# Kernel optimization log

Measured on AMD Instinct MI355X. Metric: run time of the kernel, lower is better.

The kernel has to match this reference:

```python
import jax, jax.numpy as jnp
import numpy as np

N_HEAD = 16
D_HEAD = 64


def setup_inputs() -> dict:
    key = jax.random.key(0)
    k1, k2, k3 = jax.random.split(key, 3)
    B, L, D = 2, 2048, 1024
    inp = jax.random.normal(k1, (B, L, D), dtype=jnp.float32)
    # causal mask: True -> masked (matches torch masked_fill_ semantics)
    mask = jnp.triu(jnp.ones((L, L), dtype=bool), k=1)[None, None, :, :]
    W_qkv = jax.random.normal(k2, (D, 3 * N_HEAD * D_HEAD), dtype=jnp.float32) * 0.02
    b_qkv = jnp.zeros((3 * N_HEAD * D_HEAD,), dtype=jnp.float32)
    W_out = jax.random.normal(k3, (N_HEAD * D_HEAD, D), dtype=jnp.float32) * 0.02
    b_out = jnp.zeros((D,), dtype=jnp.float32)
    return {"input": inp, "mask": mask, "W_qkv": W_qkv, "b_qkv": b_qkv,
            "W_out": W_out, "b_out": b_out}


def reference(input, mask, W_qkv, b_qkv, W_out, b_out):
    B, L, D = input.shape
    qkv = input @ W_qkv + b_qkv                       # [B, L, 3*H*Dh]
    q, k, v = jnp.split(qkv, 3, axis=-1)              # each [B, L, H*Dh]
    qh = q.reshape(B, L, N_HEAD, D_HEAD)
    kh = k.reshape(B, L, N_HEAD, D_HEAD)
    vh = v.reshape(B, L, N_HEAD, D_HEAD)
    scale = 1.0 / (D_HEAD ** 0.5)
    attn = jnp.einsum('bqhd,bkhd->bhqk', qh, kh) * scale  # [B, H, L, L]
    attn = jnp.where(mask, -jnp.inf, attn)
    attn = jax.nn.softmax(attn, axis=-1)
    out = jnp.einsum('bhqk,bkhd->bqhd', attn, vh).reshape(B, L, D)
    out = out @ W_out + b_out
    # next_memory equivalent: (k, v) pre-head-split, as in the torch code
    return (out, k, v)
```

## Files before the change

kernel.cpp:

```cpp
#include <hip/hip_runtime.h>
#include <cstdint>

#define NHEAD 16
#define DHEAD 64
#define SEQ   2048
#define DMODEL 1024
#define MTOT  4096
#define NQKV  3072

typedef __bf16 bf16x8 __attribute__((ext_vector_type(8)));
typedef short  s16x4  __attribute__((ext_vector_type(4)));
typedef float  f32x4  __attribute__((ext_vector_type(4)));

__device__ __forceinline__ unsigned short f2bf(float f) {
  union { float f; unsigned u; } v; v.f = f;
  unsigned r = v.u + 0x7fffu + ((v.u >> 16) & 1u);
  return (unsigned short)(r >> 16);
}

__device__ __forceinline__ void gl_lds16(const void* g, void* l) {
  __builtin_amdgcn_global_load_lds(
      reinterpret_cast<const __attribute__((address_space(1))) unsigned int*>(
          reinterpret_cast<uintptr_t>(g)),
      reinterpret_cast<__attribute__((address_space(3))) unsigned int*>(
          reinterpret_cast<uintptr_t>(l)),
      16, 0, 0);
}

#if __has_builtin(__builtin_amdgcn_mfma_f32_16x16x16bf16_1k)
#define MFMA_PV(a, b, c) __builtin_amdgcn_mfma_f32_16x16x16bf16_1k(a, b, c, 0, 0, 0)
#else
__device__ __forceinline__ f32x4 mfma_pv_asm(s16x4 a, s16x4 b, f32x4 c) {
  f32x4 d;
  asm volatile("v_mfma_f32_16x16x16_bf16 %0, %1, %2, %3"
               : "=v"(d) : "v"(a), "v"(b), "v"(c));
  return d;
}
#define MFMA_PV(a, b, c) mfma_pv_asm(a, b, c)
#endif

__global__ void k_prepass(const float* __restrict__ x, unsigned short* __restrict__ y,
                          const float* __restrict__ W0, unsigned short* __restrict__ T0,
                          const float* __restrict__ W1, unsigned short* __restrict__ T1) {
  __shared__ unsigned short t[32][33];
  const int bid = blockIdx.x;
  if (bid < 4096) {
    const int i = bid * 256 + threadIdx.x;
    float4 v = reinterpret_cast<const float4*>(x)[i];
    ushort4 o;
    o.x = f2bf(v.x); o.y = f2bf(v.y); o.z = f2bf(v.z); o.w = f2bf(v.w);
    reinterpret_cast<ushort4*>(y)[i] = o;
  } else {
    const int b2 = bid - 4096;
    const int bx = b2 & 127;
    const int by = b2 >> 7;
    const float* W = (bx < 96) ? W0 : W1;
    unsigned short* WT = (bx < 96) ? T0 : T1;
    const int N = (bx < 96) ? 3072 : 1024;
    const int n0 = ((bx < 96) ? bx : (bx - 96)) * 32;
    const int k0 = by * 32;
    const int tx = threadIdx.x & 31, ty = threadIdx.x >> 5;
    for (int i = ty; i < 32; i += 8)
      t[i][tx] = f2bf(W[(size_t)(k0 + i) * N + n0 + tx]);
    __syncthreads();
    for (int i = ty; i < 32; i += 8)
      WT[(size_t)(n0 + i) * 1024 + k0 + tx] = t[tx][i];
  }
}

__global__ __launch_bounds__(256, 3) void k_gemm_qkv(
    const unsigned short* __restrict__ A, const unsigned short* __restrict__ Bt,
    const float* __restrict__ bias, float* __restrict__ outbase,
    unsigned short* __restrict__ qbf, unsigned short* __restrict__ kbf,
    unsigned short* __restrict__ vtbf) {
  __shared__ __attribute__((aligned(16))) unsigned short As[2][128 * 32];
  __shared__ __attribute__((aligned(16))) unsigned short Bs[2][128 * 32];
  const int tid = threadIdx.x, lane = tid & 63;
  const int w = tid >> 6, wm = w >> 1, wn = w & 1;
  const int c = lane & 15, q = lane >> 4;
  const int kc = (c & 3) ^ ((c >> 2) & 3);
  const int bm = blockIdx.x * 128, bn = blockIdx.y * 128;
  const int srow = tid >> 2;
  const int skey = (srow & 3) ^ ((srow >> 2) & 3);
  const int scolsw = (((tid & 3) ^ skey) << 3);
  const unsigned short* Ag = A + (size_t)(bm + srow) * DMODEL + scolsw;
  const unsigned short* Bg = Bt + (size_t)(bn + srow) * DMODEL + scolsw;
  f32x4 acc[4][4] = {};

  gl_lds16(Ag, As[0] + tid * 8);
  gl_lds16(Ag + (size_t)64 * DMODEL, As[0] + 2048 + tid * 8);
  gl_lds16(Bg, Bs[0] + tid * 8);
  gl_lds16(Bg + (size_t)64 * DMODEL, Bs[0] + 2048 + tid * 8);

  for (int kt = 0; kt < 32; ++kt) {
    const int cur = kt & 1;
    __syncthreads();
    if (kt < 31) {
      const int k0 = (kt + 1) * 32;
      gl_lds16(Ag + k0, As[cur ^ 1] + tid * 8);
      gl_lds16(Ag + k0 + (size_t)64 * DMODEL, As[cur ^ 1] + 2048 + tid * 8);
      gl_lds16(Bg + k0, Bs[cur ^ 1] + tid * 8);
      gl_lds16(Bg + k0 + (size_t)64 * DMODEL, Bs[cur ^ 1] + 2048 + tid * 8);
    }
    const int ch = (q ^ kc) << 3;
    bf16x8 af[4], bfr[4];
#pragma unroll
    for (int i = 0; i < 4; ++i)
      af[i] = *reinterpret_cast<const bf16x8*>(As[cur] + (wm * 64 + i * 16 + c) * 32 + ch);
#pragma unroll
    for (int j = 0; j < 4; ++j)
      bfr[j] = *reinterpret_cast<const bf16x8*>(Bs[cur] + (wn * 64 + j * 16 + c) * 32 + ch);
#pragma unroll
    for (int i = 0; i < 4; ++i)
#pragma unroll
      for (int j = 0; j < 4; ++j)
        acc[i][j] = __builtin_amdgcn_mfma_f32_16x16x32_bf16(af[i], bfr[j], acc[i][j], 0, 0, 0);
  }

  const int sec = bn >> 10;
  if (sec == 2) {
    __syncthreads();
    char* stg = reinterpret_cast<char*>((w < 2) ? (&As[0][0] + w * 4096)
                                                : (&Bs[0][0] + (w - 2) * 4096));
#pragma unroll
    for (int j = 0; j < 4; ++j) {
      const int gn = bn + wn * 64 + j * 16 + c;
      const float bv = bias[gn];
      const int cc = gn & 1023;
      const int ln = j * 16 + c;
#pragma unroll
      for (int i = 0; i < 4; ++i) {
        const int gm0 = bm + wm * 64 + i * 16 + q * 4;
        const int lm0 = i * 16 + q * 4;
        float vals[4];
#pragma unroll
        for (int r = 0; r < 4; ++r) {
          vals[r] = acc[i][j][r] + bv;
          outbase[(size_t)8388608 + (size_t)(gm0 + r) * DMODEL + cc] = vals[r];
        }
        ushort4 tv;
        tv.x = f2bf(vals[0]); tv.y = f2bf(vals[1]);
        tv.z = f2bf(vals[2]); tv.w = f2bf(vals[3]);
        *reinterpret_cast<ushort4*>(stg + ln * 128 + ((lm0 * 2) ^ ((ln & 7) << 4))) = tv;
      }
    }
    const int gmb = bm + wm * 64;
    const int bb = gmb >> 11, tokb = gmb & 2047;
    const int hh = ((bn + wn * 64) >> 6) & 15;
    unsigned short* vrow = vtbf + ((size_t)(bb * NHEAD + hh) * DHEAD) * SEQ + tokb;
#pragma unroll
    for (int it = 0; it < 8; ++it) {
      const int r_ = (lane >> 3) + it * 8;
      const int g = lane & 7;
      const uint4 val = *reinterpret_cast<const uint4*>(
          stg + r_ * 128 + (((unsigned)g << 4) ^ ((r_ & 7) << 4)));
      *reinterpret_cast<uint4*>(vrow + (size_t)r_ * SEQ + g * 8) = val;
    }
  } else {
#pragma unroll
    for (int j = 0; j < 4; ++j) {
      const int gn = bn + wn * 64 + j * 16 + c;
      const float bv = bias[gn];
      const int cc = gn & 1023, hh = cc >> 6, dd = cc & 63;
#pragma unroll
      for (int i = 0; i < 4; ++i) {
#pragma unroll
        for (int r = 0; r < 4; ++r) {
          const int gm = bm + wm * 64 + i * 16 + q * 4 + r;
          const int bb = gm >> 11, tok = gm & 2047;
          const float val = acc[i][j][r] + bv;
          const size_t hoff = ((size_t)(bb * NHEAD + hh) * SEQ + tok) * DHEAD + dd;
          if (sec == 0) {
            qbf[hoff] = f2bf(val);
          } else {
            outbase[(size_t)4194304 + (size_t)gm * DMODEL + cc] = val;
            kbf[hoff] = f2bf(val);
          }
        }
      }
    }
  }
}

__global__ __launch_bounds__(256) void k_attn(
    const unsigned short* __restrict__ qbf, const unsigned short* __restrict__ kbf,
    const unsigned short* __restrict__ vtbf, unsigned short* __restrict__ aout) {
  __shared__ __attribute__((aligned(16))) unsigned short Ks[128 * 64];
  __shared__ __attribute__((aligned(16))) unsigned short Vs[64 * 128];

  const int tid = threadIdx.x, lane = tid & 63, w = tid >> 6;
  const int c = lane & 15, q = lane >> 4;
  const int oo = blockIdx.x >> 5, kk = oo & 7, ssl = oo >> 3;
  const int qsub = (ssl == 0) ? (31 - kk) : (ssl == 1) ? kk
                 : (ssl == 2) ? (23 - kk) : (8 + kk);
  const int bh = blockIdx.x & 31;
  const int kmax = qsub >> 1;
  const size_t hoff = (size_t)bh * SEQ * DHEAD;

  const unsigned short* qg = qbf + hoff + (size_t)(qsub * 64 + w * 16 + c) * DHEAD;
  const bf16x8 qb0 = *reinterpret_cast<const bf16x8*>(qg + q * 8);
  const bf16x8 qb1 = *reinterpret_cast<const bf16x8*>(qg + 32 + q * 8);

  f32x4 o[4] = {};
  float lpart = 0.f;
  const float sscale = 0.125f * 1.44269504088896340736f;
  const int qloc = (qsub & 1) * 64 + w * 16 + c;
  const int cx = c & 7;

  const int krow = tid >> 3, kswz = (tid & 7) ^ (krow & 7);
  const int vrow = tid >> 4, vswz = (tid & 15) ^ (vrow & 7);
  const unsigned short* kgb = kbf + hoff;
  const unsigned short* vgb = vtbf + (size_t)bh * DHEAD * SEQ;

  for (int kt = 0; kt <= kmax; ++kt) {
    __syncthreads();
    const unsigned short* kg = kgb + (size_t)kt * 128 * DHEAD;
#pragma unroll
    for (int is = 0; is < 4; ++is)
      gl_lds16(kg + (krow + is * 32) * 64 + kswz * 8, Ks + is * 2048 + tid * 8);
    const unsigned short* vg = vgb + kt * 128;
#pragma unroll
    for (int is = 0; is < 4; ++is)
      gl_lds16(vg + (size_t)(vrow + is * 16) * SEQ + vswz * 8, Vs + is * 2048 + tid * 8);
    __syncthreads();

    f32x4 s[8];
    __builtin_amdgcn_s_setprio(1);
#pragma unroll
    for (int mi = 0; mi < 8; ++mi) {
      const unsigned short* kr = Ks + (mi * 16 + c) * 64;
      const bf16x8 ak0 = *reinterpret_cast<const bf16x8*>(kr + (q ^ cx) * 8);
      const bf16x8 ak1 = *reinterpret_cast<const bf16x8*>(kr + ((4 + q) ^ cx) * 8);
      f32x4 t = {};
      t = __builtin_amdgcn_mfma_f32_16x16x32_bf16(ak0, qb0, t, 0, 0, 0);
      t = __builtin_amdgcn_mfma_f32_16x16x32_bf16(ak1, qb1, t, 0, 0, 0);
      s[mi] = t;
    }
    __builtin_amdgcn_s_setprio(0);

    if (kt == kmax) {
#pragma unroll
      for (int mi = 0; mi < 8; ++mi)
#pragma unroll
        for (int r = 0; r < 4; ++r)
          if (mi * 16 + q * 4 + r > qloc) s[mi][r] = -__builtin_inff();
    }

    s16x4 pb[8];
#pragma unroll
    for (int mi = 0; mi < 8; ++mi) {
      const float p0 = __builtin_amdgcn_exp2f(s[mi][0] * sscale);
      const float p1 = __builtin_amdgcn_exp2f(s[mi][1] * sscale);
      const float p2 = __builtin_amdgcn_exp2f(s[mi][2] * sscale);
      const float p3 = __builtin_amdgcn_exp2f(s[mi][3] * sscale);
      lpart += (p0 + p1) + (p2 + p3);
      union { s16x4 v; unsigned u[2]; } pk;
      pk.u[0] = __builtin_amdgcn_perm(__float_as_uint(p1), __float_as_uint(p0), 0x07060302u);
      pk.u[1] = __builtin_amdgcn_perm(__float_as_uint(p3), __float_as_uint(p2), 0x07060302u);
      pb[mi] = pk.v;
    }

    __builtin_amdgcn_s_setprio(1);
#pragma unroll
    for (int dm = 0; dm < 4; ++dm) {
      const unsigned short* vr = Vs + (dm * 16 + c) * 128 + (q & 1) * 4;
#pragma unroll
      for (int kf = 0; kf < 8; ++kf) {
        const s16x4 av = *reinterpret_cast<const s16x4*>(
            vr + (((kf * 2 + (q >> 1)) ^ cx) * 8));
        o[dm] = MFMA_PV(av, pb[kf], o[dm]);
      }
    }
    __builtin_amdgcn_s_setprio(0);
  }

  float lrun = lpart;
  lrun += __shfl_xor(lrun, 16);
  lrun += __shfl_xor(lrun, 32);

  const float linv = 1.0f / lrun;
  unsigned short* Ws = Ks + w * 1024;
#pragma unroll
  for (int dm = 0; dm < 4; ++dm) {
    ushort4 ov;
    ov.x = f2bf(o[dm][0] * linv);
    ov.y = f2bf(o[dm][1] * linv);
    ov.z = f2bf(o[dm][2] * linv);
    ov.w = f2bf(o[dm][3] * linv);
    const int bofs = c * 128 + ((dm * 32 + q * 8) ^ ((c & 7) << 4));
    *reinterpret_cast<ushort4*>(Ws + (bofs >> 1)) = ov;
  }
  const int b = bh >> 4, h = bh & 15;
#pragma unroll
  for (int it = 0; it < 2; ++it) {
    const int r_ = (lane >> 3) + it * 8;
    const int g = lane & 7;
    const uint4 val = *reinterpret_cast<const uint4*>(
        Ws + ((r_ * 128 + (((unsigned)g ^ (r_ & 7)) << 4)) >> 1));
    const int row = b * SEQ + qsub * 64 + w * 16 + r_;
    *reinterpret_cast<uint4*>(aout + (size_t)row * DMODEL + h * 64 + g * 8) = val;
  }
}

__global__ __launch_bounds__(256) void k_gemm_out(
    const unsigned short* __restrict__ A, const unsigned short* __restrict__ Bt,
    const float* __restrict__ bias, float* __restrict__ C) {
  __shared__ __attribute__((aligned(16))) unsigned short As[2][128 * 32];
  __shared__ __attribute__((aligned(16))) unsigned short Bs[2][64 * 32];
  const int tid = threadIdx.x, lane = tid & 63;
  const int w = tid >> 6, wm = w >> 1, wn = w & 1;
  const int c = lane & 15, q = lane >> 4;
  const int kc = (c & 3) ^ ((c >> 2) & 3);
  const int bm = blockIdx.x * 128, bn = blockIdx.y * 64;
  const int srow = tid >> 2;
  const int skey = (srow & 3) ^ ((srow >> 2) & 3);
  const int scolsw = (((tid & 3) ^ skey) << 3);
  const unsigned short* Ag = A + (size_t)(bm + srow) * DMODEL + scolsw;
  const unsigned short* Bg = Bt + (size_t)(bn + srow) * DMODEL + scolsw;
  f32x4 acc[4][2] = {};

  gl_lds16(Ag, As[0] + tid * 8);
  gl_lds16(Ag + (size_t)64 * DMODEL, As[0] + 2048 + tid * 8);
  gl_lds16(Bg, Bs[0] + tid * 8);

  for (int kt = 0; kt < 32; ++kt) {
    const int cur = kt & 1;
    __syncthreads();
    if (kt < 31) {
      const int k0 = (kt + 1) * 32;
      gl_lds16(Ag + k0, As[cur ^ 1] + tid * 8);
      gl_lds16(Ag + k0 + (size_t)64 * DMODEL, As[cur ^ 1] + 2048 + tid * 8);
      gl_lds16(Bg + k0, Bs[cur ^ 1] + tid * 8);
    }
    const int ch = (q ^ kc) << 3;
    bf16x8 af[4], bfr[2];
#pragma unroll
    for (int i = 0; i < 4; ++i)
      af[i] = *reinterpret_cast<const bf16x8*>(As[cur] + (wm * 64 + i * 16 + c) * 32 + ch);
#pragma unroll
    for (int j = 0; j < 2; ++j)
      bfr[j] = *reinterpret_cast<const bf16x8*>(Bs[cur] + (wn * 32 + j * 16 + c) * 32 + ch);
#pragma unroll
    for (int i = 0; i < 4; ++i)
#pragma unroll
      for (int j = 0; j < 2; ++j)
        acc[i][j] = __builtin_amdgcn_mfma_f32_16x16x32_bf16(af[i], bfr[j], acc[i][j], 0, 0, 0);
  }

#pragma unroll
  for (int j = 0; j < 2; ++j) {
    const int gn = bn + wn * 32 + j * 16 + c;
    const float bv = bias[gn];
#pragma unroll
    for (int i = 0; i < 4; ++i)
#pragma unroll
      for (int r = 0; r < 4; ++r) {
        const int gm = bm + wm * 64 + i * 16 + q * 4 + r;
        C[(size_t)gm * DMODEL + gn] = acc[i][j][r] + bv;
      }
  }
}

extern "C" void kernel_launch(void* const* d_in, const int* in_sizes, int n_in,
                              void* d_out, int out_size, void* d_ws, size_t ws_size,
                              hipStream_t stream) {
  (void)in_sizes; (void)n_in; (void)out_size; (void)ws_size;
  const float* input = (const float*)d_in[0];
  const float* W_qkv = (const float*)d_in[2];
  const float* b_qkv = (const float*)d_in[3];
  const float* W_out = (const float*)d_in[4];
  const float* b_out = (const float*)d_in[5];
  float* out = (float*)d_out;

  unsigned char* ws = (unsigned char*)d_ws;
  unsigned short* Abf   = (unsigned short*)(ws + 0);
  unsigned short* WqkvT = (unsigned short*)(ws + 8388608);
  unsigned short* WoutT = (unsigned short*)(ws + 14680064);
  unsigned short* Qbf   = (unsigned short*)(ws + 16777216);
  unsigned short* Kbf   = (unsigned short*)(ws + 25165824);
  unsigned short* VTbf  = (unsigned short*)(ws + 33554432);
  unsigned short* Aout  = (unsigned short*)(ws + 41943040);

  k_prepass<<<8192, 256, 0, stream>>>(input, Abf, W_qkv, WqkvT, W_out, WoutT);
  k_gemm_qkv<<<dim3(32, 24), 256, 0, stream>>>(Abf, WqkvT, b_qkv, out, Qbf, Kbf, VTbf);
  k_attn<<<1024, 256, 0, stream>>>(Qbf, Kbf, VTbf, Aout);
  k_gemm_out<<<dim3(32, 16), 256, 0, stream>>>(Aout, WoutT, b_out, out);
}
```

Before: 188.6 us.

## Pair mirrored causal query tiles per attention block to share K/V loads

```diff
diff --git a/kernel.cpp b/kernel.cpp
--- a/kernel.cpp
+++ b/kernel.cpp
@@ -38,6 +38,8 @@
 }
 #define MFMA_PV(a, b, c) mfma_pv_asm(a, b, c)
 #endif
+
+#define QSCALE 0.18033688011112042f
 
 __global__ void k_prepass(const float* __restrict__ x, unsigned short* __restrict__ y,
                           const float* __restrict__ W0, unsigned short* __restrict__ T0,
@@ -171,7 +173,7 @@
           const float val = acc[i][j][r] + bv;
           const size_t hoff = ((size_t)(bb * NHEAD + hh) * SEQ + tok) * DHEAD + dd;
           if (sec == 0) {
-            qbf[hoff] = f2bf(val);
+            qbf[hoff] = f2bf(val * QSCALE);
           } else {
             outbase[(size_t)4194304 + (size_t)gm * DMODEL + cc] = val;
             kbf[hoff] = f2bf(val);
@@ -190,21 +192,23 @@
 
   const int tid = threadIdx.x, lane = tid & 63, w = tid >> 6;
   const int c = lane & 15, q = lane >> 4;
-  const int oo = blockIdx.x >> 5, kk = oo & 7, ssl = oo >> 3;
-  const int qsub = (ssl == 0) ? (31 - kk) : (ssl == 1) ? kk
-                 : (ssl == 2) ? (23 - kk) : (8 + kk);
   const int bh = blockIdx.x & 31;
-  const int kmax = qsub >> 1;
+  const int jj = blockIdx.x >> 5;
+  const int qa = 31 - jj, qb = jj;
+  const int ka = qa >> 1, kb = qb >> 1;
   const size_t hoff = (size_t)bh * SEQ * DHEAD;
 
-  const unsigned short* qg = qbf + hoff + (size_t)(qsub * 64 + w * 16 + c) * DHEAD;
-  const bf16x8 qb0 = *reinterpret_cast<const bf16x8*>(qg + q * 8);
-  const bf16x8 qb1 = *reinterpret_cast<const bf16x8*>(qg + 32 + q * 8);
-
-  f32x4 o[4] = {};
-  float lpart = 0.f;
-  const float sscale = 0.125f * 1.44269504088896340736f;
-  const int qloc = (qsub & 1) * 64 + w * 16 + c;
+  const unsigned short* qga = qbf + hoff + (size_t)(qa * 64 + w * 16 + c) * DHEAD;
+  const bf16x8 qA0 = *reinterpret_cast<const bf16x8*>(qga + q * 8);
+  const bf16x8 qA1 = *reinterpret_cast<const bf16x8*>(qga + 32 + q * 8);
+  const unsigned short* qgb = qbf + hoff + (size_t)(qb * 64 + w * 16 + c) * DHEAD;
+  const bf16x8 qB0 = *reinterpret_cast<const bf16x8*>(qgb + q * 8);
+  const bf16x8 qB1 = *reinterpret_cast<const bf16x8*>(qgb + 32 + q * 8);
+
+  f32x4 oa[4] = {}, ob[4] = {};
+  float lpa = 0.f, lpb = 0.f;
+  const int qloca = (qa & 1) * 64 + w * 16 + c;
+  const int qlocb = (qb & 1) * 64 + w * 16 + c;
   const int cx = c & 7;
 
   const int krow = tid >> 3, kswz = (tid & 7) ^ (krow & 7);
@@ -212,7 +216,7 @@
   const unsigned short* kgb = kbf + hoff;
   const unsigned short* vgb = vtbf + (size_t)bh * DHEAD * SEQ;
 
-  for (int kt = 0; kt <= kmax; ++kt) {
+  for (int kt = 0; kt <= ka; ++kt) {
     __syncthreads();
     const unsigned short* kg = kgb + (size_t)kt * 128 * DHEAD;
 #pragma unroll
@@ -224,81 +228,160 @@
       gl_lds16(vg + (size_t)(vrow + is * 16) * SEQ + vswz * 8, Vs + is * 2048 + tid * 8);
     __syncthreads();
 
-    f32x4 s[8];
-    __builtin_amdgcn_s_setprio(1);
-#pragma unroll
-    for (int mi = 0; mi < 8; ++mi) {
-      const unsigned short* kr = Ks + (mi * 16 + c) * 64;
-      const bf16x8 ak0 = *reinterpret_cast<const bf16x8*>(kr + (q ^ cx) * 8);
-      const bf16x8 ak1 = *reinterpret_cast<const bf16x8*>(kr + ((4 + q) ^ cx) * 8);
-      f32x4 t = {};
-      t = __builtin_amdgcn_mfma_f32_16x16x32_bf16(ak0, qb0, t, 0, 0, 0);
-      t = __builtin_amdgcn_mfma_f32_16x16x32_bf16(ak1, qb1, t, 0, 0, 0);
-      s[mi] = t;
-    }
-    __builtin_amdgcn_s_setprio(0);
-
-    if (kt == kmax) {
-#pragma unroll
-      for (int mi = 0; mi < 8; ++mi)
-#pragma unroll
-        for (int r = 0; r < 4; ++r)
-          if (mi * 16 + q * 4 + r > qloc) s[mi][r] = -__builtin_inff();
-    }
-
-    s16x4 pb[8];
-#pragma unroll
-    for (int mi = 0; mi < 8; ++mi) {
-      const float p0 = __builtin_amdgcn_exp2f(s[mi][0] * sscale);
-      const float p1 = __builtin_amdgcn_exp2f(s[mi][1] * sscale);
-      const float p2 = __builtin_amdgcn_exp2f(s[mi][2] * sscale);
-      const float p3 = __builtin_amdgcn_exp2f(s[mi][3] * sscale);
-      lpart += (p0 + p1) + (p2 + p3);
-      union { s16x4 v; unsigned u[2]; } pk;
-      pk.u[0] = __builtin_amdgcn_perm(__float_as_uint(p1), __float_as_uint(p0), 0x07060302u);
-      pk.u[1] = __builtin_amdgcn_perm(__float_as_uint(p3), __float_as_uint(p2), 0x07060302u);
-      pb[mi] = pk.v;
-    }
-
-    __builtin_amdgcn_s_setprio(1);
+    {
+      f32x4 s[8];
+      __builtin_amdgcn_s_setprio(1);
+#pragma unroll
+      for (int mi = 0; mi < 8; ++mi) {
+        const unsigned short* kr = Ks + (mi * 16 + c) * 64;
+        const bf16x8 ak0 = *reinterpret_cast<const bf16x8*>(kr + (q ^ cx) * 8);
+        const bf16x8 ak1 = *reinterpret_cast<const bf16x8*>(kr + ((4 + q) ^ cx) * 8);
+        f32x4 t = {};
+        t = __builtin_amdgcn_mfma_f32_16x16x32_bf16(ak0, qA0, t, 0, 0, 0);
+        t = __builtin_amdgcn_mfma_f32_16x16x32_bf16(ak1, qA1, t, 0, 0, 0);
+        s[mi] = t;
+      }
+      __builtin_amdgcn_s_setprio(0);
+
+      if (kt == ka) {
+#pragma unroll
+        for (int mi = 0; mi < 8; ++mi)
+#pragma unroll
+          for (int r = 0; r < 4; ++r)
+            if (mi * 16 + q * 4 + r > qloca) s[mi][r] = -__builtin_inff();
+      }
+
+      s16x4 pb[8];
+#pragma unroll
+      for (int mi = 0; mi < 8; ++mi) {
+        const float p0 = __builtin_amdgcn_exp2f(s[mi][0]);
+        const float p1 = __builtin_amdgcn_exp2f(s[mi][1]);
+        const float p2 = __builtin_amdgcn_exp2f(s[mi][2]);
+        const float p3 = __builtin_amdgcn_exp2f(s[mi][3]);
+        lpa += (p0 + p1) + (p2 + p3);
+        union { s16x4 v; unsigned u[2]; } pk;
+        pk.u[0] = __builtin_amdgcn_perm(__float_as_uint(p1), __float_as_uint(p0), 0x07060302u);
+        pk.u[1] = __builtin_amdgcn_perm(__float_as_uint(p3), __float_as_uint(p2), 0x07060302u);
+        pb[mi] = pk.v;
+      }
+
+      __builtin_amdgcn_s_setprio(1);
+#pragma unroll
+      for (int dm = 0; dm < 4; ++dm) {
+        const unsigned short* vr = Vs + (dm * 16 + c) * 128 + (q & 1) * 4;
+#pragma unroll
+        for (int kf = 0; kf < 8; ++kf) {
+          const s16x4 av = *reinterpret_cast<const s16x4*>(
+              vr + (((kf * 2 + (q >> 1)) ^ cx) * 8));
+          oa[dm] = MFMA_PV(av, pb[kf], oa[dm]);
+        }
+      }
+      __builtin_amdgcn_s_setprio(0);
+    }
+
+    if (kt <= kb) {
+      f32x4 s[8];
+      __builtin_amdgcn_s_setprio(1);
+#pragma unroll
+      for (int mi = 0; mi < 8; ++mi) {
+        const unsigned short* kr = Ks + (mi * 16 + c) * 64;
+        const bf16x8 ak0 = *reinterpret_cast<const bf16x8*>(kr + (q ^ cx) * 8);
+        const bf16x8 ak1 = *reinterpret_cast<const bf16x8*>(kr + ((4 + q) ^ cx) * 8);
+        f32x4 t = {};
+        t = __builtin_amdgcn_mfma_f32_16x16x32_bf16(ak0, qB0, t, 0, 0, 0);
+        t = __builtin_amdgcn_mfma_f32_16x16x32_bf16(ak1, qB1, t, 0, 0, 0);
+        s[mi] = t;
+      }
+      __builtin_amdgcn_s_setprio(0);
+
+      if (kt == kb) {
+#pragma unroll
+        for (int mi = 0; mi < 8; ++mi)
+#pragma unroll
+          for (int r = 0; r < 4; ++r)
+            if (mi * 16 + q * 4 + r > qlocb) s[mi][r] = -__builtin_inff();
+      }
+
+      s16x4 pb[8];
+#pragma unroll
+      for (int mi = 0; mi < 8; ++mi) {
+        const float p0 = __builtin_amdgcn_exp2f(s[mi][0]);
+        const float p1 = __builtin_amdgcn_exp2f(s[mi][1]);
+        const float p2 = __builtin_amdgcn_exp2f(s[mi][2]);
+        const float p3 = __builtin_amdgcn_exp2f(s[mi][3]);
+        lpb += (p0 + p1) + (p2 + p3);
+        union { s16x4 v; unsigned u[2]; } pk;
+        pk.u[0] = __builtin_amdgcn_perm(__float_as_uint(p1), __float_as_uint(p0), 0x07060302u);
+        pk.u[1] = __builtin_amdgcn_perm(__float_as_uint(p3), __float_as_uint(p2), 0x07060302u);
+        pb[mi] = pk.v;
+      }
+
+      __builtin_amdgcn_s_setprio(1);
+#pragma unroll
+      for (int dm = 0; dm < 4; ++dm) {
+        const unsigned short* vr = Vs + (dm * 16 + c) * 128 + (q & 1) * 4;
+#pragma unroll
+        for (int kf = 0; kf < 8; ++kf) {
+          const s16x4 av = *reinterpret_cast<const s16x4*>(
+              vr + (((kf * 2 + (q >> 1)) ^ cx) * 8));
+          ob[dm] = MFMA_PV(av, pb[kf], ob[dm]);
+        }
+      }
+      __builtin_amdgcn_s_setprio(0);
+    }
+  }
+
+  float la = lpa; la += __shfl_xor(la, 16); la += __shfl_xor(la, 32);
+  float lb = lpb; lb += __shfl_xor(lb, 16); lb += __shfl_xor(lb, 32);
+
+  __syncthreads();
+  const int bidx = bh >> 4, h = bh & 15;
+
+  {
+    const float linv = 1.0f / la;
+    unsigned short* Ws = Ks + w * 2048;
 #pragma unroll
     for (int dm = 0; dm < 4; ++dm) {
-      const unsigned short* vr = Vs + (dm * 16 + c) * 128 + (q & 1) * 4;
-#pragma unroll
-      for (int kf = 0; kf < 8; ++kf) {
-        const s16x4 av = *reinterpret_cast<const s16x4*>(
-            vr + (((kf * 2 + (q >> 1)) ^ cx) * 8));
-        o[dm] = MFMA_PV(av, pb[kf], o[dm]);
-      }
-    }
-    __builtin_amdgcn_s_setprio(0);
-  }
-
-  float lrun = lpart;
-  lrun += __shfl_xor(lrun, 16);
-  lrun += __shfl_xor(lrun, 32);
-
-  const float linv = 1.0f / lrun;
-  unsigned short* Ws = Ks + w * 1024;
-#pragma unroll
-  for (int dm = 0; dm < 4; ++dm) {
-    ushort4 ov;
-    ov.x = f2bf(o[dm][0] * linv);
-    ov.y = f2bf(o[dm][1] * linv);
-    ov.z = f2bf(o[dm][2] * linv);
-    ov.w = f2bf(o[dm][3] * linv);
-    const int bofs = c * 128 + ((dm * 32 + q * 8) ^ ((c & 7) << 4));
-    *reinterpret_cast<ushort4*>(Ws + (bofs >> 1)) = ov;
-  }
-  const int b = bh >> 4, h = bh & 15;
-#pragma unroll
-  for (int it = 0; it < 2; ++it) {
-    const int r_ = (lane >> 3) + it * 8;
-    const int g = lane & 7;
-    const uint4 val = *reinterpret_cast<const uint4*>(
-        Ws + ((r_ * 128 + (((unsigned)g ^ (r_ & 7)) << 4)) >> 1));
-    const int row = b * SEQ + qsub * 64 + w * 16 + r_;
-    *reinterpret_cast<uint4*>(aout + (size_t)row * DMODEL + h * 64 + g * 8) = val;
+      ushort4 ov;
+      ov.x = f2bf(oa[dm][0] * linv);
+      ov.y = f2bf(oa[dm][1] * linv);
+      ov.z = f2bf(oa[dm][2] * linv);
+      ov.w = f2bf(oa[dm][3] * linv);
+      const int bofs = c * 128 + ((dm * 32 + q * 8) ^ ((c & 7) << 4));
+      *reinterpret_cast<ushort4*>(Ws + (bofs >> 1)) = ov;
+    }
+#pragma unroll
+    for (int it = 0; it < 2; ++it) {
+      const int r_ = (lane >> 3) + it * 8;
+      const int g = lane & 7;
+      const uint4 val = *reinterpret_cast<const uint4*>(
+          Ws + ((r_ * 128 + (((unsigned)g ^ (r_ & 7)) << 4)) >> 1));
+      const int row = bidx * SEQ + qa * 64 + w * 16 + r_;
+      *reinterpret_cast<uint4*>(aout + (size_t)row * DMODEL + h * 64 + g * 8) = val;
+    }
+  }
+  {
+    const float linv = 1.0f / lb;
+    unsigned short* Ws = Ks + w * 2048 + 1024;
+#pragma unroll
+    for (int dm = 0; dm < 4; ++dm) {
+      ushort4 ov;
+      ov.x = f2bf(ob[dm][0] * linv);
+      ov.y = f2bf(ob[dm][1] * linv);
+      ov.z = f2bf(ob[dm][2] * linv);
+      ov.w = f2bf(ob[dm][3] * linv);
+      const int bofs = c * 128 + ((dm * 32 + q * 8) ^ ((c & 7) << 4));
+      *reinterpret_cast<ushort4*>(Ws + (bofs >> 1)) = ov;
+    }
+#pragma unroll
+    for (int it = 0; it < 2; ++it) {
+      const int r_ = (lane >> 3) + it * 8;
+      const int g = lane & 7;
+      const uint4 val = *reinterpret_cast<const uint4*>(
+          Ws + ((r_ * 128 + (((unsigned)g ^ (r_ & 7)) << 4)) >> 1));
+      const int row = bidx * SEQ + qb * 64 + w * 16 + r_;
+      *reinterpret_cast<uint4*>(aout + (size_t)row * DMODEL + h * 64 + g * 8) = val;
+    }
   }
 }
 
@@ -383,6 +466,6 @@
 
   k_prepass<<<8192, 256, 0, stream>>>(input, Abf, W_qkv, WqkvT, W_out, WoutT);
   k_gemm_qkv<<<dim3(32, 24), 256, 0, stream>>>(Abf, WqkvT, b_qkv, out, Qbf, Kbf, VTbf);
-  k_attn<<<1024, 256, 0, stream>>>(Qbf, Kbf, VTbf, Aout);
+  k_attn<<<512, 256, 0, stream>>>(Qbf, Kbf, VTbf, Aout);
   k_gemm_out<<<dim3(32, 16), 256, 0, stream>>>(Aout, WoutT, b_out, out);
 }
```

Result: no change. 191.3 us (+1.4%).
